# Optimization experiments

Hardware: AMD Instinct MI355X
Metric: run time of the kernel (lower is better)

## Reference

```python
import jax, jax.numpy as jnp
import numpy as np

N, E, G = 50000, 1600000, 512
H, NF_IN, NF_OUT, GF_OUT, EDIM, DEPTH = 128, 64, 64, 128, 16, 3
EPS = 1e-5


def seg_softmax(logits, seg, num):
    m = jax.ops.segment_max(logits, seg, num_segments=num)
    e = jnp.exp(logits - m[seg])
    s = jax.ops.segment_sum(e, seg, num_segments=num)
    return e / s[seg]


def batchnorm_train(x, gamma, beta):
    mu = jnp.mean(x, axis=0)
    var = jnp.mean((x - mu) ** 2, axis=0)  # biased, as torch BN training
    return (x - mu) * jax.lax.rsqrt(var + EPS) * gamma + beta


def setup_inputs() -> dict:
    key = jax.random.key(0)
    ks = jax.random.split(key, 20)
    inp = {}
    inp['x'] = jax.random.normal(ks[0], (N, NF_IN), jnp.float32)
    inp['edge_index'] = jax.random.randint(ks[1], (2, E), 0, N, jnp.int64)
    inp['edge_attr'] = jax.random.normal(ks[2], (E, EDIM), jnp.float32)
    inp['batch'] = jnp.sort(jax.random.randint(ks[3], (N,), 0, G, jnp.int64))
    inp['num_graphs'] = G
    s = 0.05
    inp['Wi'] = jax.random.normal(ks[4], (H, NF_IN), jnp.float32) * s
    inp['bi'] = jnp.zeros((H,), jnp.float32)
    inp['gat_W'] = jax.random.normal(ks[5], (DEPTH, H, 2 * H), jnp.float32) * s
    inp['gat_a'] = jax.random.normal(ks[6], (DEPTH, 2 * H), jnp.float32) * s
    inp['nfW1'] = jax.random.normal(ks[7], (H, H), jnp.float32) * s
    inp['nfb1'] = jnp.zeros((H,), jnp.float32)
    inp['nf_g'] = jnp.ones((H,), jnp.float32)
    inp['nf_b'] = jnp.zeros((H,), jnp.float32)
    inp['nfW2'] = jax.random.normal(ks[8], (NF_OUT, H), jnp.float32) * s
    inp['nfb2'] = jnp.zeros((NF_OUT,), jnp.float32)
    inp['gfW1'] = jax.random.normal(ks[9], (H, H), jnp.float32) * s
    inp['gfb1'] = jnp.zeros((H,), jnp.float32)
    inp['gf_g'] = jnp.ones((H,), jnp.float32)
    inp['gf_b'] = jnp.zeros((H,), jnp.float32)
    inp['gfW2'] = jax.random.normal(ks[10], (GF_OUT, H), jnp.float32) * s
    inp['gfb2'] = jnp.zeros((GF_OUT,), jnp.float32)
    return inp


def reference(x, edge_index, edge_attr, batch, num_graphs, Wi, bi, gat_W, gat_a,
              nfW1, nfb1, nf_g, nf_b, nfW2, nfb2,
              gfW1, gfb1, gf_g, gf_b, gfW2, gfb2):
    src, dst = edge_index[0], edge_index[1]
    nf = x @ Wi.T + bi  # [N,H]
    for i in range(DEPTH):
        src_nf = nf[src]            # [E,H]
        dst_nf = nf[dst]            # [E,H]
        ef = jnp.concatenate([src_nf, dst_nf], axis=-1) @ gat_a[i]  # [E]
        alpha = seg_softmax(ef, dst, N)
        agg = jax.ops.segment_sum(alpha[:, None] * src_nf, dst, num_segments=N)
        nf = jax.nn.relu(jnp.concatenate([nf, agg], axis=-1) @ gat_W[i].T)
    # 3-iteration attention pooling over graphs
    h = nf
    for _ in range(3):
        logits = jnp.sum(h * nf, axis=-1)  # [N]
        alpha = seg_softmax(logits, batch, num_graphs)
        h = alpha[:, None] * nf
    gf = jax.ops.segment_sum(h, batch, num_segments=num_graphs)  # [G,H]
    nf_out = jax.nn.relu(batchnorm_train(nf @ nfW1.T + nfb1, nf_g, nf_b)) @ nfW2.T + nfb2
    gf_out = jax.nn.relu(batchnorm_train(gf @ gfW1.T + gfb1, gf_g, gf_b)) @ gfW2.T + gfb2
    return nf_out, edge_attr, gf_out
```

## Files before the change

### kernel.cpp

```cpp
#include <hip/hip_runtime.h>

#define NN 50000
#define NE 1600000
#define NG 512
#define HD 128
#define NGRP 8
#define GRPSZ ((NN + NGRP - 1) / NGRP)
#define PCAP 28672

typedef __attribute__((ext_vector_type(8))) short bf16x8;
typedef __attribute__((ext_vector_type(4))) float f32x4;

static __device__ __forceinline__ unsigned bf16rn(float x) {
  unsigned b = __float_as_uint(x);
  return (b + 0x7FFFu + ((b >> 16) & 1u)) >> 16;
}
static __device__ __forceinline__ float bf16tof(unsigned short u) {
  return __uint_as_float(((unsigned)u) << 16);
}

__global__ void __launch_bounds__(256) k_part(const int* __restrict__ src,
                                              const int* __restrict__ dst,
                                              uint2* __restrict__ pairs,
                                              int* __restrict__ pcnt) {
  __shared__ uint2 buf[8][512];
  __shared__ int lcnt[8];
  __shared__ int gbase[8];
  __shared__ int nfl[8];
  const int tid = threadIdx.x;
  const int b = blockIdx.x & 7;
  if (tid < 8) lcnt[tid] = 0;
  __syncthreads();
  const int stride = gridDim.x * 256;
  for (int base_e = blockIdx.x * 256; base_e < NE; base_e += stride) {
    int e = base_e + tid;
    bool valid = e < NE;
    if (valid) {
      int d = dst[e];
      int s = src[e];
      int g = d / GRPSZ;
      int pos = atomicAdd(&lcnt[g], 1);
      buf[g][pos] = make_uint2((unsigned)d, (unsigned)s);
    }
    __syncthreads();
    if (tid < 8) {
      int c = lcnt[tid];
      int nf = (c >= 256) ? 256 : 0;
      nfl[tid] = nf;
      gbase[tid] = nf ? atomicAdd(&pcnt[tid * 8 + b], nf) : 0;
    }
    __syncthreads();
#pragma unroll
    for (int g0 = 0; g0 < 8; ++g0) {
      if (nfl[g0]) {
        int gb = gbase[g0] + tid;
        if (gb < PCAP)
          pairs[(size_t)(g0 * 8 + b) * PCAP + gb] = buf[g0][tid];
      }
    }
    __syncthreads();
#pragma unroll
    for (int g0 = 0; g0 < 8; ++g0) {
      if (nfl[g0]) {
        int rem = lcnt[g0] - 256;
        if (tid < rem) buf[g0][tid] = buf[g0][256 + tid];
      }
    }
    __syncthreads();
    if (tid < 8 && nfl[tid]) lcnt[tid] -= 256;
    __syncthreads();
  }
  if (tid < 8) {
    int c = lcnt[tid];
    gbase[tid] = c ? atomicAdd(&pcnt[tid * 8 + b], c) : 0;
  }
  __syncthreads();
#pragma unroll
  for (int g0 = 0; g0 < 8; ++g0) {
    int c = lcnt[g0];
    if (tid < c) {
      int gb = gbase[g0] + tid;
      if (gb < PCAP)
        pairs[(size_t)(g0 * 8 + b) * PCAP + gb] = buf[g0][tid];
    }
  }
}

__global__ void __launch_bounds__(256) k_hist(const uint2* __restrict__ pairs,
                                              const int* __restrict__ pcnt,
                                              int* __restrict__ hcnt) {
  __shared__ int hist[GRPSZ];
  const int b = blockIdx.x;
  const int g = b & 7, sub = b >> 3;
  const int li = g * 8 + sub;
  const int lo = g * GRPSZ;
  for (int i = threadIdx.x; i < GRPSZ; i += 256) hist[i] = 0;
  __syncthreads();
  int cnt = min(pcnt[li], PCAP);
  const uint2* lst = pairs + (size_t)li * PCAP;
  for (int i = threadIdx.x; i < cnt; i += 256)
    atomicAdd(&hist[(int)lst[i].x - lo], 1);
  __syncthreads();
  for (int i = threadIdx.x; i < GRPSZ; i += 256)
    hcnt[(size_t)li * GRPSZ + i] = hist[i];
}

__global__ void k_degsum(const int* __restrict__ hcnt, int* __restrict__ deg) {
  int d = blockIdx.x * 256 + threadIdx.x;
  if (d >= NN) return;
  int g = d / GRPSZ, i = d - g * GRPSZ;
  int s = 0;
#pragma unroll
  for (int sub = 0; sub < 8; ++sub) s += hcnt[(size_t)(g * 8 + sub) * GRPSZ + i];
  deg[d] = s;
}

__global__ void __launch_bounds__(256) k_scat3(const uint2* __restrict__ pairs,
                                               const int* __restrict__ pcnt,
                                               const int* __restrict__ hcnt,
                                               const int* __restrict__ row_ptr,
                                               int* __restrict__ csr_src) {
  __shared__ int cur[GRPSZ];
  const int b = blockIdx.x;
  const int g = b & 7, sub = b >> 3;
  const int li = g * 8 + sub;
  const int lo = g * GRPSZ;
  for (int i = threadIdx.x; i < GRPSZ; i += 256) {
    int base = row_ptr[lo + i];
    for (int s2 = 0; s2 < sub; ++s2)
      base += hcnt[(size_t)(g * 8 + s2) * GRPSZ + i];
    cur[i] = base;
  }
  __syncthreads();
  int cnt = min(pcnt[li], PCAP);
  const uint2* lst = pairs + (size_t)li * PCAP;
  for (int i = threadIdx.x; i < cnt; i += 256) {
    uint2 p = lst[i];
    int pos = atomicAdd(&cur[(int)p.x - lo], 1);
    csr_src[pos] = (int)p.y;
  }
}

__global__ void k_scan_block(const int* __restrict__ in, int* __restrict__ out,
                             int* __restrict__ bsum, int n) {
  __shared__ int tmp[1024];
  int i = blockIdx.x * 1024 + threadIdx.x;
  int v = (i < n) ? in[i] : 0;
  tmp[threadIdx.x] = v;
  __syncthreads();
  for (int off = 1; off < 1024; off <<= 1) {
    int t = (threadIdx.x >= (unsigned)off) ? tmp[threadIdx.x - off] : 0;
    __syncthreads();
    tmp[threadIdx.x] += t;
    __syncthreads();
  }
  if (i < n) out[i] = tmp[threadIdx.x] - v;
  if (threadIdx.x == 1023 && bsum) bsum[blockIdx.x] = tmp[1023];
}

__global__ void k_scan_small(int* __restrict__ a, int n) {
  __shared__ int tmp[1024];
  int v = ((int)threadIdx.x < n) ? a[threadIdx.x] : 0;
  tmp[threadIdx.x] = v;
  __syncthreads();
  for (int off = 1; off < 1024; off <<= 1) {
    int t = (threadIdx.x >= (unsigned)off) ? tmp[threadIdx.x - off] : 0;
    __syncthreads();
    tmp[threadIdx.x] += t;
    __syncthreads();
  }
  if ((int)threadIdx.x < n) a[threadIdx.x] = tmp[threadIdx.x] - v;
}

__global__ void k_scan_add(int* __restrict__ out, const int* __restrict__ bsum, int n) {
  int i = blockIdx.x * 1024 + threadIdx.x;
  if (i < n) out[i] += bsum[blockIdx.x];
  if (blockIdx.x == 0 && threadIdx.x == 0) out[n] = NE;
}

__global__ void k_init_bounds(int* __restrict__ gs, int* __restrict__ ge) {
  int g = blockIdx.x * 256 + threadIdx.x;
  if (g < NG) { gs[g] = NN; ge[g] = 0; }
}
__global__ void k_bounds(const int* __restrict__ batch, int* __restrict__ gs, int* __restrict__ ge) {
  int n = blockIdx.x * 256 + threadIdx.x;
  if (n < NN) {
    int b = batch[n];
    atomicMin(&gs[b], n);
    atomicMax(&ge[b], n + 1);
  }
}

__global__ void k_cvt(const float* __restrict__ a, unsigned short* __restrict__ b, int n) {
  int i = blockIdx.x * 256 + threadIdx.x;
  if (i < n) b[i] = (unsigned short)bf16rn(a[i]);
}

__global__ void k_gat_agg(const unsigned* __restrict__ nf16, const float* __restrict__ e1,
                          const int* __restrict__ row_ptr, const int* __restrict__ csr_src,
                          unsigned short* __restrict__ agg16) {
  int node = blockIdx.x * 4 + (threadIdx.x >> 6);
  int lane = threadIdx.x & 63;
  if (node >= NN) return;
  int s = row_ptr[node], e = row_ptr[node + 1];
  const int q = lane >> 4;
  const int c = lane & 15;

  float acc[8];
#pragma unroll
  for (int i = 0; i < 8; ++i) acc[i] = 0.f;
  float zloc = 0.f;

  int jj = s + q;
  bool v0 = jj < e;
  int sc = v0 ? csr_src[jj] : 0;
  float w = v0 ? e1[sc] : 0.f;
  uint4 u = *(const uint4*)(nf16 + (size_t)sc * 64 + c * 4);

  for (int j = s; j < e; j += 4) {
    int jn = j + 4 + q;
    bool vn = jn < e;
    int scn = vn ? csr_src[jn] : 0;
    float wn = vn ? e1[scn] : 0.f;
    uint4 un = *(const uint4*)(nf16 + (size_t)scn * 64 + c * 4);
    zloc += w;
    acc[0] = fmaf(w, __uint_as_float(u.x << 16), acc[0]);
    acc[1] = fmaf(w, __uint_as_float(u.x & 0xFFFF0000u), acc[1]);
    acc[2] = fmaf(w, __uint_as_float(u.y << 16), acc[2]);
    acc[3] = fmaf(w, __uint_as_float(u.y & 0xFFFF0000u), acc[3]);
    acc[4] = fmaf(w, __uint_as_float(u.z << 16), acc[4]);
    acc[5] = fmaf(w, __uint_as_float(u.z & 0xFFFF0000u), acc[5]);
    acc[6] = fmaf(w, __uint_as_float(u.w << 16), acc[6]);
    acc[7] = fmaf(w, __uint_as_float(u.w & 0xFFFF0000u), acc[7]);
    sc = scn; w = wn; u = un;
  }

  zloc += __shfl_xor(zloc, 16);
  zloc += __shfl_xor(zloc, 32);
  float inv = (zloc > 0.f) ? 1.f / zloc : 0.f;
#pragma unroll
  for (int i = 0; i < 8; ++i) {
    acc[i] += __shfl_xor(acc[i], 16);
    acc[i] += __shfl_xor(acc[i], 32);
    acc[i] *= inv;
  }
  if (q == 0) {
    uint4 pk;
    pk.x = bf16rn(acc[0]) | (bf16rn(acc[1]) << 16);
    pk.y = bf16rn(acc[2]) | (bf16rn(acc[3]) << 16);
    pk.z = bf16rn(acc[4]) | (bf16rn(acc[5]) << 16);
    pk.w = bf16rn(acc[6]) | (bf16rn(acc[7]) << 16);
    *(uint4*)(agg16 + (size_t)node * HD + c * 8) = pk;
  }
}

template <int K, int KA, int HO, bool RELUOUT, bool BIAS, bool OUTF32, bool OUT16, int DOTM>
__global__ void __launch_bounds__(256) k_mfma(
    const unsigned short* __restrict__ A1, const unsigned short* __restrict__ A2,
    const unsigned short* __restrict__ W16, const float* __restrict__ bias,
    float* __restrict__ outf, unsigned short* __restrict__ out16,
    const float* __restrict__ dvec, float* __restrict__ dout, int nrows) {
  constexpr int NT = HO / 16;
  const int l = threadIdx.x & 63;
  const int w = threadIdx.x >> 6;
  const int lr = l & 15;
  const int q = l >> 4;
  const int row0 = blockIdx.x * 64 + w * 16;
  const int arow = min(row0 + lr, nrows - 1);
  const unsigned short* pa1 = A1 + (size_t)arow * KA;
  const unsigned short* pa2 = (KA < K) ? (A2 + (size_t)arow * (K - KA)) : nullptr;

  f32x4 acc[NT];
#pragma unroll
  for (int t = 0; t < NT; ++t) acc[t] = (f32x4){0.f, 0.f, 0.f, 0.f};

#pragma unroll
  for (int s = 0; s < K / 32; ++s) {
    const int kg = s * 32 + q * 8;
    bf16x8 af;
    if constexpr (KA == K) {
      af = *(const bf16x8*)(pa1 + kg);
    } else {
      af = (s * 32 < KA) ? *(const bf16x8*)(pa1 + kg)
                         : *(const bf16x8*)(pa2 + (kg - KA));
    }
#pragma unroll
    for (int t = 0; t < NT; ++t) {
      bf16x8 bfr = *(const bf16x8*)(W16 + (size_t)(t * 16 + lr) * K + kg);
      acc[t] = __builtin_amdgcn_mfma_f32_16x16x32_bf16(af, bfr, acc[t], 0, 0, 0);
    }
  }

  float bv[BIAS ? NT : 1];
  if constexpr (BIAS) {
#pragma unroll
    for (int t = 0; t < NT; ++t) bv[t] = bias[t * 16 + lr];
  }
  float dv[DOTM == 1 ? NT : 1];
  if constexpr (DOTM == 1) {
#pragma unroll
    for (int t = 0; t < NT; ++t) dv[t] = dvec[t * 16 + lr];
  }
  float p[4] = {0.f, 0.f, 0.f, 0.f};
#pragma unroll
  for (int j = 0; j < 4; ++j) {
    int n = row0 + q * 4 + j;
    bool ok = n < nrows;
#pragma unroll
    for (int t = 0; t < NT; ++t) {
      float v = acc[t][j];
      if constexpr (BIAS) v += bv[t];
      if constexpr (RELUOUT) v = fmaxf(v, 0.f);
      if (ok) {
        if constexpr (OUTF32) outf[(size_t)n * HO + t * 16 + lr] = v;
        if constexpr (OUT16) out16[(size_t)n * HO + t * 16 + lr] = (unsigned short)bf16rn(v);
      }
      if constexpr (DOTM == 1) p[j] = fmaf(v, dv[t], p[j]);
      if constexpr (DOTM == 2) p[j] = fmaf(v, v, p[j]);
    }
  }
  if constexpr (DOTM != 0) {
#pragma unroll
    for (int j = 0; j < 4; ++j) {
      p[j] += __shfl_xor(p[j], 1);
      p[j] += __shfl_xor(p[j], 2);
      p[j] += __shfl_xor(p[j], 4);
      p[j] += __shfl_xor(p[j], 8);
    }
    if (lr == 0) {
#pragma unroll
      for (int j = 0; j < 4; ++j) {
        int n = row0 + q * 4 + j;
        if (n < nrows) dout[n] = (DOTM == 1) ? __expf(p[j]) : p[j];
      }
    }
  }
}

template <int K, int KA, int HO, bool PRE, bool RELUOUT, bool BIAS, bool OUT16, int DOTM>
__global__ void __launch_bounds__(256) k_gemm(
    const float* __restrict__ inA, const float* __restrict__ inB,
    const float* __restrict__ W, const float* __restrict__ bias,
    const float* __restrict__ preA, const float* __restrict__ preB,
    float* __restrict__ out, int nrows,
    unsigned* __restrict__ out16, const float* __restrict__ dvec,
    float* __restrict__ dout) {
  constexpr int KC = 64;
  constexpr int BM = 64;
  constexpr int MT = 4;
  constexpr int NT = HO / 16;
  constexpr int LDW = HO + 4;
  constexpr int LDA = KC + 4;

  __shared__ float Wl[KC * LDW];
  __shared__ float inl[BM * LDA];

  const int tid = threadIdx.x;
  const int tr = tid >> 4;
  const int tc = tid & 15;
  const int row0 = blockIdx.x * BM;
  const int r0 = tr * MT;
  const int c0 = tc * NT;

  float acc[MT][NT];
#pragma unroll
  for (int i = 0; i < MT; ++i)
#pragma unroll
    for (int j = 0; j < NT; ++j) acc[i][j] = BIAS ? bias[c0 + j] : 0.f;

  for (int cc = 0; cc < K / KC; ++cc) {
    const int k0 = cc * KC;
    if (cc) __syncthreads();
    for (int idx = tid; idx < HO * (KC / 4); idx += 256) {
      int h = idx >> 4;
      int qq = idx & 15;
      float4 w = *(const float4*)(W + (size_t)h * K + k0 + qq * 4);
      Wl[(qq * 4 + 0) * LDW + h] = w.x;
      Wl[(qq * 4 + 1) * LDW + h] = w.y;
      Wl[(qq * 4 + 2) * LDW + h] = w.z;
      Wl[(qq * 4 + 3) * LDW + h] = w.w;
    }
    for (int idx = tid; idx < BM * (KC / 4); idx += 256) {
      int r = idx >> 4;
      int qq = idx & 15;
      int n = row0 + r;
      int kg = k0 + qq * 4;
      float4 v = make_float4(0.f, 0.f, 0.f, 0.f);
      if (n < nrows) {
        if constexpr (KA == K) {
          v = *(const float4*)(inA + (size_t)n * K + kg);
        } else {
          if (k0 < KA) v = *(const float4*)(inA + (size_t)n * KA + kg);
          else         v = *(const float4*)(inB + (size_t)n * (K - KA) + kg - KA);
        }
      }
      if constexpr (PRE) {
        v.x = fmaxf(v.x * preA[kg + 0] + preB[kg + 0], 0.f);
        v.y = fmaxf(v.y * preA[kg + 1] + preB[kg + 1], 0.f);
        v.z = fmaxf(v.z * preA[kg + 2] + preB[kg + 2], 0.f);
        v.w = fmaxf(v.w * preA[kg + 3] + preB[kg + 3], 0.f);
      }
      *(float4*)(inl + r * LDA + qq * 4) = v;
    }
    __syncthreads();
#pragma unroll 8
    for (int k = 0; k < KC; ++k) {
      float a[MT];
#pragma unroll
      for (int i = 0; i < MT; ++i) a[i] = inl[(r0 + i) * LDA + k];
      float4 b0 = *(const float4*)(Wl + k * LDW + c0);
#pragma unroll
      for (int i = 0; i < MT; ++i) {
        acc[i][0] = fmaf(a[i], b0.x, acc[i][0]);
        acc[i][1] = fmaf(a[i], b0.y, acc[i][1]);
        acc[i][2] = fmaf(a[i], b0.z, acc[i][2]);
        acc[i][3] = fmaf(a[i], b0.w, acc[i][3]);
      }
      if constexpr (NT == 8) {
        float4 b1 = *(const float4*)(Wl + k * LDW + c0 + 4);
#pragma unroll
        for (int i = 0; i < MT; ++i) {
          acc[i][4] = fmaf(a[i], b1.x, acc[i][4]);
          acc[i][5] = fmaf(a[i], b1.y, acc[i][5]);
          acc[i][6] = fmaf(a[i], b1.z, acc[i][6]);
          acc[i][7] = fmaf(a[i], b1.w, acc[i][7]);
        }
      }
    }
  }
  float dv[DOTM == 1 ? NT : 1];
  if constexpr (DOTM == 1) {
#pragma unroll
    for (int j = 0; j < NT; ++j) dv[j] = dvec[c0 + j];
  }
#pragma unroll
  for (int i = 0; i < MT; ++i) {
    int n = row0 + r0 + i;
    if constexpr (RELUOUT) {
#pragma unroll
      for (int j = 0; j < NT; ++j) acc[i][j] = fmaxf(acc[i][j], 0.f);
    }
    if (n < nrows) {
      float4 o0 = make_float4(acc[i][0], acc[i][1], acc[i][2], acc[i][3]);
      *(float4*)(out + (size_t)n * HO + c0) = o0;
      if constexpr (NT == 8) {
        float4 o1 = make_float4(acc[i][4], acc[i][5], acc[i][6], acc[i][7]);
        *(float4*)(out + (size_t)n * HO + c0 + 4) = o1;
      }
      if constexpr (OUT16 && NT == 8) {
        uint4 pk;
        pk.x = bf16rn(acc[i][0]) | (bf16rn(acc[i][1]) << 16);
        pk.y = bf16rn(acc[i][2]) | (bf16rn(acc[i][3]) << 16);
        pk.z = bf16rn(acc[i][4]) | (bf16rn(acc[i][5]) << 16);
        pk.w = bf16rn(acc[i][6]) | (bf16rn(acc[i][7]) << 16);
        *(uint4*)(out16 + (size_t)n * 64 + tc * 4) = pk;
      }
    }
    if constexpr (DOTM != 0) {
      float p = 0.f;
#pragma unroll
      for (int j = 0; j < NT; ++j)
        p = fmaf(acc[i][j], (DOTM == 1) ? dv[j] : acc[i][j], p);
      p += __shfl_xor(p, 1);
      p += __shfl_xor(p, 2);
      p += __shfl_xor(p, 4);
      p += __shfl_xor(p, 8);
      if (tc == 0 && n < nrows) dout[n] = (DOTM == 1) ? __expf(p) : p;
    }
  }
}

__global__ void k_pool(const unsigned short* __restrict__ nf16, const float* __restrict__ r,
                       const int* __restrict__ gs, const int* __restrict__ ge,
                       float* __restrict__ alpha, float* __restrict__ gf) {
  int g = blockIdx.x;
  int s = gs[g], e = ge[g];
  __shared__ float red[256];
  for (int it = 0; it < 3; ++it) {
    float lm = -INFINITY;
    for (int n = s + threadIdx.x; n < e; n += 256) {
      float l = r[n];
      if (it) l *= alpha[n];
      lm = fmaxf(lm, l);
    }
    red[threadIdx.x] = lm;
    __syncthreads();
    for (int off = 128; off > 0; off >>= 1) {
      if ((int)threadIdx.x < off) red[threadIdx.x] = fmaxf(red[threadIdx.x], red[threadIdx.x + off]);
      __syncthreads();
    }
    float m = red[0];
    __syncthreads();
    float zz = 0.f;
    for (int n = s + threadIdx.x; n < e; n += 256) {
      float l = r[n];
      if (it) l *= alpha[n];
      zz += __expf(l - m);
    }
    red[threadIdx.x] = zz;
    __syncthreads();
    for (int off = 128; off > 0; off >>= 1) {
      if ((int)threadIdx.x < off) red[threadIdx.x] += red[threadIdx.x + off];
      __syncthreads();
    }
    float z = red[0];
    __syncthreads();
    float invz = 1.f / z;
    for (int n = s + threadIdx.x; n < e; n += 256) {
      float l = r[n];
      if (it) l *= alpha[n];
      alpha[n] = __expf(l - m) * invz;
    }
    __syncthreads();
  }
  int c = threadIdx.x & 127;
  int rr2 = threadIdx.x >> 7;
  float acc = 0.f;
  for (int n = s + rr2; n < e; n += 2)
    acc += alpha[n] * bf16tof(nf16[(size_t)n * HD + c]);
  red[threadIdx.x] = acc;
  __syncthreads();
  if (rr2 == 0) gf[(size_t)g * HD + c] = red[threadIdx.x] + red[threadIdx.x + 128];
}

__global__ void k_colstats(const float* __restrict__ y, float* __restrict__ sum,
                           float* __restrict__ sumsq, int R, int CH) {
  int c = threadIdx.x & 127;
  int rr = threadIdx.x >> 7;
  int r0 = blockIdx.x * CH;
  int r1 = min(R, r0 + CH);
  float s = 0.f, q = 0.f;
  for (int r = r0 + rr; r < r1; r += 2) {
    float v = y[(size_t)r * HD + c];
    s += v;
    q += v * v;
  }
  __shared__ float ls[256], lq[256];
  ls[threadIdx.x] = s;
  lq[threadIdx.x] = q;
  __syncthreads();
  if (rr == 0) {
    s += ls[threadIdx.x + 128];
    q += lq[threadIdx.x + 128];
    atomicAdd(&sum[c], s);
    atomicAdd(&sumsq[c], q);
  }
}

__global__ void k_bn_final(const float* __restrict__ sum, const float* __restrict__ sumsq,
                           const float* __restrict__ g, const float* __restrict__ b,
                           float* __restrict__ A, float* __restrict__ B, float R) {
  int c = threadIdx.x;
  float mu = sum[c] / R;
  float var = sumsq[c] / R - mu * mu;
  float a = g[c] * rsqrtf(var + 1e-5f);
  A[c] = a;
  B[c] = b[c] - mu * a;
}

__global__ void k_bnapply(const float* __restrict__ y, const float* __restrict__ Ac,
                          const float* __restrict__ Bc, unsigned short* __restrict__ z) {
  int i = blockIdx.x * 256 + threadIdx.x;
  if (i >= NN * 16) return;
  int c = (i & 15) * 8;
  const float4* yp = (const float4*)y + (size_t)i * 2;
  float4 v0 = yp[0], v1 = yp[1];
  float4 a0 = *(const float4*)(Ac + c), a1 = *(const float4*)(Ac + c + 4);
  float4 b0 = *(const float4*)(Bc + c), b1 = *(const float4*)(Bc + c + 4);
  float r0 = fmaxf(fmaf(v0.x, a0.x, b0.x), 0.f);
  float r1 = fmaxf(fmaf(v0.y, a0.y, b0.y), 0.f);
  float r2 = fmaxf(fmaf(v0.z, a0.z, b0.z), 0.f);
  float r3 = fmaxf(fmaf(v0.w, a0.w, b0.w), 0.f);
  float r4 = fmaxf(fmaf(v1.x, a1.x, b1.x), 0.f);
  float r5 = fmaxf(fmaf(v1.y, a1.y, b1.y), 0.f);
  float r6 = fmaxf(fmaf(v1.z, a1.z, b1.z), 0.f);
  float r7 = fmaxf(fmaf(v1.w, a1.w, b1.w), 0.f);
  uint4 pk;
  pk.x = bf16rn(r0) | (bf16rn(r1) << 16);
  pk.y = bf16rn(r2) | (bf16rn(r3) << 16);
  pk.z = bf16rn(r4) | (bf16rn(r5) << 16);
  pk.w = bf16rn(r6) | (bf16rn(r7) << 16);
  *(uint4*)(z + (size_t)i * 8) = pk;
}

__global__ void k_copy4(const float4* __restrict__ a, float4* __restrict__ b, int n) {
  int i = blockIdx.x * 256 + threadIdx.x;
  if (i < n) b[i] = a[i];
}

extern "C" void kernel_launch(void* const* d_in, const int* in_sizes, int n_in,
                              void* d_out, int out_size, void* d_ws, size_t ws_size,
                              hipStream_t stream) {
  const float* x        = (const float*)d_in[0];
  const int*   ei       = (const int*)d_in[1];
  const float* edge_attr= (const float*)d_in[2];
  const int*   batch    = (const int*)d_in[3];
  const float* Wi       = (const float*)d_in[5];
  const float* bi       = (const float*)d_in[6];
  const float* gat_W    = (const float*)d_in[7];
  const float* gat_a    = (const float*)d_in[8];
  const float* nfW1     = (const float*)d_in[9];
  const float* nfb1     = (const float*)d_in[10];
  const float* nf_g     = (const float*)d_in[11];
  const float* nf_b     = (const float*)d_in[12];
  const float* nfW2     = (const float*)d_in[13];
  const float* nfb2     = (const float*)d_in[14];
  const float* gfW1     = (const float*)d_in[15];
  const float* gfb1     = (const float*)d_in[16];
  const float* gf_g     = (const float*)d_in[17];
  const float* gf_b     = (const float*)d_in[18];
  const float* gfW2     = (const float*)d_in[19];
  const float* gfb2     = (const float*)d_in[20];

  float* out = (float*)d_out;

  unsigned short* nf16A = (unsigned short*)d_ws;
  unsigned short* nf16B = nf16A + (size_t)NN * HD;
  unsigned short* agg16 = nf16B + (size_t)NN * HD;
  unsigned short* z16   = agg16 + (size_t)NN * HD;
  unsigned short* wt_gat = z16 + (size_t)NN * HD;
  unsigned short* wt_nf1 = wt_gat + 3 * 128 * 256;
  unsigned short* wt_nf2 = wt_nf1 + 128 * 128;
  float* nfA   = (float*)(wt_nf2 + 64 * 128);
  float* e1v   = nfA + (size_t)NN * HD;
  float* rv    = e1v + NN;
  float* alpha = rv + NN;
  float* gf    = alpha + NN;
  float* gy    = gf + (size_t)NG * HD;
  float* sums  = gy + (size_t)NG * HD;
  int* deg     = (int*)(sums + 512);
  int* row_ptr = deg + NN;
  int* csr_src = row_ptr + NN + 1;
  int* bsum    = csr_src + NE;
  int* gs      = bsum + 64;
  int* ge      = gs + NG;
  int* pcnt    = ge + NG;
  int* hcnt    = pcnt + 64;
  uint2* pairs = (uint2*)nfA;

  const int* src  = ei;
  const int* dstp = ei + NE;

  hipMemsetAsync(pcnt, 0, 64 * sizeof(int), stream);
  k_part<<<512, 256, 0, stream>>>(src, dstp, pairs, pcnt);
  k_hist<<<64, 256, 0, stream>>>(pairs, pcnt, hcnt);
  k_degsum<<<(NN + 255) / 256, 256, 0, stream>>>(hcnt, deg);
  int nsb = (NN + 1023) / 1024;
  k_scan_block<<<nsb, 1024, 0, stream>>>(deg, row_ptr, bsum, NN);
  k_scan_small<<<1, 1024, 0, stream>>>(bsum, nsb);
  k_scan_add<<<nsb, 1024, 0, stream>>>(row_ptr, bsum, NN);
  k_scat3<<<64, 256, 0, stream>>>(pairs, pcnt, hcnt, row_ptr, csr_src);

  k_init_bounds<<<2, 256, 0, stream>>>(gs, ge);
  k_bounds<<<(NN + 255) / 256, 256, 0, stream>>>(batch, gs, ge);

  k_cvt<<<(3 * 128 * 256 + 255) / 256, 256, 0, stream>>>(gat_W, wt_gat, 3 * 128 * 256);
  k_cvt<<<(128 * 128 + 255) / 256, 256, 0, stream>>>(nfW1, wt_nf1, 128 * 128);
  k_cvt<<<(64 * 128 + 255) / 256, 256, 0, stream>>>(nfW2, wt_nf2, 64 * 128);

  k_gemm<64, 64, 128, false, false, true, true, 1><<<(NN + 63) / 64, 256, 0, stream>>>(
      x, nullptr, Wi, bi, nullptr, nullptr, nfA, NN, (unsigned*)nf16A, gat_a, e1v);

  unsigned short* cur = nf16A;
  unsigned short* nxt = nf16B;
  const int gemm_grid = (NN + 63) / 64;
  for (int l = 0; l < 3; ++l) {
    k_gat_agg<<<(NN + 3) / 4, 256, 0, stream>>>((const unsigned*)cur, e1v, row_ptr, csr_src, agg16);
    if (l < 2) {
      k_mfma<256, 128, 128, true, false, false, true, 1><<<gemm_grid, 256, 0, stream>>>(
          cur, agg16, wt_gat + (size_t)l * 128 * 256, nullptr,
          nullptr, nxt, gat_a + (size_t)(l + 1) * 256, e1v, NN);
    } else {
      k_mfma<256, 128, 128, true, false, false, true, 2><<<gemm_grid, 256, 0, stream>>>(
          cur, agg16, wt_gat + (size_t)l * 128 * 256, nullptr,
          nullptr, nxt, nullptr, rv, NN);
    }
    unsigned short* t = cur; cur = nxt; nxt = t;
  }

  k_pool<<<NG, 256, 0, stream>>>(cur, rv, gs, ge, alpha, gf);

  k_mfma<128, 128, 128, false, true, true, false, 0><<<gemm_grid, 256, 0, stream>>>(
      cur, nullptr, wt_nf1, nfb1, nfA, nullptr, nullptr, nullptr, NN);
  hipMemsetAsync(sums, 0, 256 * sizeof(float), stream);
  k_colstats<<<200, 256, 0, stream>>>(nfA, sums, sums + 128, NN, 250);
  k_bn_final<<<1, 128, 0, stream>>>(sums, sums + 128, nf_g, nf_b, sums + 256, sums + 384, (float)NN);
  k_bnapply<<<(NN * 16 + 255) / 256, 256, 0, stream>>>(nfA, sums + 256, sums + 384, z16);
  k_mfma<128, 128, 64, false, true, true, false, 0><<<gemm_grid, 256, 0, stream>>>(
      z16, nullptr, wt_nf2, nfb2, out, nullptr, nullptr, nullptr, NN);

  k_gemm<128, 128, 128, false, false, true, false, 0><<<(NG + 63) / 64, 256, 0, stream>>>(
      gf, nullptr, gfW1, gfb1, nullptr, nullptr, gy, NG, nullptr, nullptr, nullptr);
  hipMemsetAsync(sums, 0, 256 * sizeof(float), stream);
  k_colstats<<<4, 256, 0, stream>>>(gy, sums, sums + 128, NG, 128);
  k_bn_final<<<1, 128, 0, stream>>>(sums, sums + 128, gf_g, gf_b, sums + 256, sums + 384, (float)NG);
  k_gemm<128, 128, 128, true, false, true, false, 0><<<(NG + 63) / 64, 256, 0, stream>>>(
      gy, nullptr, gfW2, gfb2, sums + 256, sums + 384,
      out + (size_t)NN * 64 + (size_t)NE * 16, NG, nullptr, nullptr, nullptr);

  int n4 = NE * 16 / 4;
  k_copy4<<<(n4 + 255) / 256, 256, 0, stream>>>((const float4*)edge_attr,
                                                (float4*)(out + (size_t)NN * 64), n4);
}
```

Before: 674.0 us.

## Fuse CSR scan into scatter, merge weight conversions, widen GAT aggregation lanes

Replaces the degree-sum, three-stage scan and scatter kernels with one k_csr kernel. Each block computes its group's prefix offsets locally from pcnt and hcnt and writes row_ptr itself. The three weight conversion launches are merged into one kernel, and the separate BN sums memsets are folded into the single initial memset by giving the node and graph BN their own sum buffers. k_gat_agg now has each lane handle 16 features across 8 edges in parallel instead of 8 features across 4 edges, which raises memory-level parallelism per wave. The cost is more registers and some serial per-thread scanning work inside k_csr.

```diff
diff --git a/kernel.cpp b/kernel.cpp
--- a/kernel.cpp
+++ b/kernel.cpp
@@ -105,32 +105,55 @@
     hcnt[(size_t)li * GRPSZ + i] = hist[i];
 }
 
-__global__ void k_degsum(const int* __restrict__ hcnt, int* __restrict__ deg) {
-  int d = blockIdx.x * 256 + threadIdx.x;
-  if (d >= NN) return;
-  int g = d / GRPSZ, i = d - g * GRPSZ;
-  int s = 0;
-#pragma unroll
-  for (int sub = 0; sub < 8; ++sub) s += hcnt[(size_t)(g * 8 + sub) * GRPSZ + i];
-  deg[d] = s;
-}
-
-__global__ void __launch_bounds__(256) k_scat3(const uint2* __restrict__ pairs,
-                                               const int* __restrict__ pcnt,
-                                               const int* __restrict__ hcnt,
-                                               const int* __restrict__ row_ptr,
-                                               int* __restrict__ csr_src) {
+__global__ void __launch_bounds__(256) k_csr(const uint2* __restrict__ pairs,
+                                             const int* __restrict__ pcnt,
+                                             const int* __restrict__ hcnt,
+                                             int* __restrict__ row_ptr,
+                                             int* __restrict__ csr_src) {
+  __shared__ int rp[GRPSZ];
   __shared__ int cur[GRPSZ];
+  __shared__ int wsum[256];
   const int b = blockIdx.x;
   const int g = b & 7, sub = b >> 3;
   const int li = g * 8 + sub;
   const int lo = g * GRPSZ;
+  int gbase = 0;
+  for (int gg = 0; gg < g; ++gg)
+#pragma unroll
+    for (int ss = 0; ss < 8; ++ss) gbase += pcnt[gg * 8 + ss];
   for (int i = threadIdx.x; i < GRPSZ; i += 256) {
-    int base = row_ptr[lo + i];
-    for (int s2 = 0; s2 < sub; ++s2)
-      base += hcnt[(size_t)(g * 8 + s2) * GRPSZ + i];
-    cur[i] = base;
-  }
+    int dsum = 0, before = 0;
+#pragma unroll
+    for (int ss = 0; ss < 8; ++ss) {
+      int h = hcnt[(size_t)(g * 8 + ss) * GRPSZ + i];
+      dsum += h;
+      if (ss < sub) before += h;
+    }
+    rp[i] = dsum;
+    cur[i] = before;
+  }
+  __syncthreads();
+  const int CH = (GRPSZ + 255) / 256;
+  int t0 = threadIdx.x * CH;
+  int t1 = min(GRPSZ, t0 + CH);
+  int s = 0;
+  for (int i = t0; i < t1; ++i) { int v = rp[i]; rp[i] = s; s += v; }
+  wsum[threadIdx.x] = s;
+  __syncthreads();
+  for (int off = 1; off < 256; off <<= 1) {
+    int t = ((int)threadIdx.x >= off) ? wsum[threadIdx.x - off] : 0;
+    __syncthreads();
+    wsum[threadIdx.x] += t;
+    __syncthreads();
+  }
+  int add = gbase + ((threadIdx.x > 0) ? wsum[threadIdx.x - 1] : 0);
+  for (int i = t0; i < t1; ++i) rp[i] += add;
+  __syncthreads();
+  for (int i = threadIdx.x; i < GRPSZ; i += 256) {
+    cur[i] += rp[i];
+    if (sub == 0) row_ptr[lo + i] = rp[i];
+  }
+  if (sub == 0 && g == 7 && threadIdx.x == 0) row_ptr[NN] = NE;
   __syncthreads();
   int cnt = min(pcnt[li], PCAP);
   const uint2* lst = pairs + (size_t)li * PCAP;
@@ -141,43 +164,6 @@
   }
 }
 
-__global__ void k_scan_block(const int* __restrict__ in, int* __restrict__ out,
-                             int* __restrict__ bsum, int n) {
-  __shared__ int tmp[1024];
-  int i = blockIdx.x * 1024 + threadIdx.x;
-  int v = (i < n) ? in[i] : 0;
-  tmp[threadIdx.x] = v;
-  __syncthreads();
-  for (int off = 1; off < 1024; off <<= 1) {
-    int t = (threadIdx.x >= (unsigned)off) ? tmp[threadIdx.x - off] : 0;
-    __syncthreads();
-    tmp[threadIdx.x] += t;
-    __syncthreads();
-  }
-  if (i < n) out[i] = tmp[threadIdx.x] - v;
-  if (threadIdx.x == 1023 && bsum) bsum[blockIdx.x] = tmp[1023];
-}
-
-__global__ void k_scan_small(int* __restrict__ a, int n) {
-  __shared__ int tmp[1024];
-  int v = ((int)threadIdx.x < n) ? a[threadIdx.x] : 0;
-  tmp[threadIdx.x] = v;
-  __syncthreads();
-  for (int off = 1; off < 1024; off <<= 1) {
-    int t = (threadIdx.x >= (unsigned)off) ? tmp[threadIdx.x - off] : 0;
-    __syncthreads();
-    tmp[threadIdx.x] += t;
-    __syncthreads();
-  }
-  if ((int)threadIdx.x < n) a[threadIdx.x] = tmp[threadIdx.x] - v;
-}
-
-__global__ void k_scan_add(int* __restrict__ out, const int* __restrict__ bsum, int n) {
-  int i = blockIdx.x * 1024 + threadIdx.x;
-  if (i < n) out[i] += bsum[blockIdx.x];
-  if (blockIdx.x == 0 && threadIdx.x == 0) out[n] = NE;
-}
-
 __global__ void k_init_bounds(int* __restrict__ gs, int* __restrict__ ge) {
   int g = blockIdx.x * 256 + threadIdx.x;
   if (g < NG) { gs[g] = NN; ge[g] = 0; }
@@ -191,66 +177,89 @@
   }
 }
 
-__global__ void k_cvt(const float* __restrict__ a, unsigned short* __restrict__ b, int n) {
+__global__ void k_cvt3(const float* __restrict__ a0, int n0,
+                       const float* __restrict__ a1, int n1,
+                       const float* __restrict__ a2, int n2,
+                       unsigned short* __restrict__ b) {
   int i = blockIdx.x * 256 + threadIdx.x;
-  if (i < n) b[i] = (unsigned short)bf16rn(a[i]);
-}
-
-__global__ void k_gat_agg(const unsigned* __restrict__ nf16, const float* __restrict__ e1,
+  if (i >= n0 + n1 + n2) return;
+  float v = (i < n0) ? a0[i] : (i < n0 + n1) ? a1[i - n0] : a2[i - n0 - n1];
+  b[i] = (unsigned short)bf16rn(v);
+}
+
+__global__ void k_gat_agg(const uint4* __restrict__ nf16u4, const float* __restrict__ e1,
                           const int* __restrict__ row_ptr, const int* __restrict__ csr_src,
                           unsigned short* __restrict__ agg16) {
   int node = blockIdx.x * 4 + (threadIdx.x >> 6);
   int lane = threadIdx.x & 63;
   if (node >= NN) return;
   int s = row_ptr[node], e = row_ptr[node + 1];
-  const int q = lane >> 4;
-  const int c = lane & 15;
-
-  float acc[8];
-#pragma unroll
-  for (int i = 0; i < 8; ++i) acc[i] = 0.f;
+  const int q = lane >> 3;
+  const int c = lane & 7;
+
+  float acc[16];
+#pragma unroll
+  for (int i = 0; i < 16; ++i) acc[i] = 0.f;
   float zloc = 0.f;
 
   int jj = s + q;
   bool v0 = jj < e;
   int sc = v0 ? csr_src[jj] : 0;
   float w = v0 ? e1[sc] : 0.f;
-  uint4 u = *(const uint4*)(nf16 + (size_t)sc * 64 + c * 4);
-
-  for (int j = s; j < e; j += 4) {
-    int jn = j + 4 + q;
+  uint4 u0 = nf16u4[(size_t)sc * 16 + c * 2];
+  uint4 u1 = nf16u4[(size_t)sc * 16 + c * 2 + 1];
+
+  for (int j = s; j < e; j += 8) {
+    int jn = j + 8 + q;
     bool vn = jn < e;
     int scn = vn ? csr_src[jn] : 0;
     float wn = vn ? e1[scn] : 0.f;
-    uint4 un = *(const uint4*)(nf16 + (size_t)scn * 64 + c * 4);
+    uint4 un0 = nf16u4[(size_t)scn * 16 + c * 2];
+    uint4 un1 = nf16u4[(size_t)scn * 16 + c * 2 + 1];
     zloc += w;
-    acc[0] = fmaf(w, __uint_as_float(u.x << 16), acc[0]);
-    acc[1] = fmaf(w, __uint_as_float(u.x & 0xFFFF0000u), acc[1]);
-    acc[2] = fmaf(w, __uint_as_float(u.y << 16), acc[2]);
-    acc[3] = fmaf(w, __uint_as_float(u.y & 0xFFFF0000u), acc[3]);
-    acc[4] = fmaf(w, __uint_as_float(u.z << 16), acc[4]);
-    acc[5] = fmaf(w, __uint_as_float(u.z & 0xFFFF0000u), acc[5]);
-    acc[6] = fmaf(w, __uint_as_float(u.w << 16), acc[6]);
-    acc[7] = fmaf(w, __uint_as_float(u.w & 0xFFFF0000u), acc[7]);
-    sc = scn; w = wn; u = un;
-  }
-
+    acc[0]  = fmaf(w, __uint_as_float(u0.x << 16), acc[0]);
+    acc[1]  = fmaf(w, __uint_as_float(u0.x & 0xFFFF0000u), acc[1]);
+    acc[2]  = fmaf(w, __uint_as_float(u0.y << 16), acc[2]);
+    acc[3]  = fmaf(w, __uint_as_float(u0.y & 0xFFFF0000u), acc[3]);
+    acc[4]  = fmaf(w, __uint_as_float(u0.z << 16), acc[4]);
+    acc[5]  = fmaf(w, __uint_as_float(u0.z & 0xFFFF0000u), acc[5]);
+    acc[6]  = fmaf(w, __uint_as_float(u0.w << 16), acc[6]);
+    acc[7]  = fmaf(w, __uint_as_float(u0.w & 0xFFFF0000u), acc[7]);
+    acc[8]  = fmaf(w, __uint_as_float(u1.x << 16), acc[8]);
+    acc[9]  = fmaf(w, __uint_as_float(u1.x & 0xFFFF0000u), acc[9]);
+    acc[10] = fmaf(w, __uint_as_float(u1.y << 16), acc[10]);
+    acc[11] = fmaf(w, __uint_as_float(u1.y & 0xFFFF0000u), acc[11]);
+    acc[12] = fmaf(w, __uint_as_float(u1.z << 16), acc[12]);
+    acc[13] = fmaf(w, __uint_as_float(u1.z & 0xFFFF0000u), acc[13]);
+    acc[14] = fmaf(w, __uint_as_float(u1.w << 16), acc[14]);
+    acc[15] = fmaf(w, __uint_as_float(u1.w & 0xFFFF0000u), acc[15]);
+    sc = scn; w = wn; u0 = un0; u1 = un1;
+  }
+
+  zloc += __shfl_xor(zloc, 8);
   zloc += __shfl_xor(zloc, 16);
   zloc += __shfl_xor(zloc, 32);
   float inv = (zloc > 0.f) ? 1.f / zloc : 0.f;
 #pragma unroll
-  for (int i = 0; i < 8; ++i) {
+  for (int i = 0; i < 16; ++i) {
+    acc[i] += __shfl_xor(acc[i], 8);
     acc[i] += __shfl_xor(acc[i], 16);
     acc[i] += __shfl_xor(acc[i], 32);
     acc[i] *= inv;
   }
   if (q == 0) {
-    uint4 pk;
-    pk.x = bf16rn(acc[0]) | (bf16rn(acc[1]) << 16);
-    pk.y = bf16rn(acc[2]) | (bf16rn(acc[3]) << 16);
-    pk.z = bf16rn(acc[4]) | (bf16rn(acc[5]) << 16);
-    pk.w = bf16rn(acc[6]) | (bf16rn(acc[7]) << 16);
-    *(uint4*)(agg16 + (size_t)node * HD + c * 8) = pk;
+    uint4 p0, p1;
+    p0.x = bf16rn(acc[0])  | (bf16rn(acc[1])  << 16);
+    p0.y = bf16rn(acc[2])  | (bf16rn(acc[3])  << 16);
+    p0.z = bf16rn(acc[4])  | (bf16rn(acc[5])  << 16);
+    p0.w = bf16rn(acc[6])  | (bf16rn(acc[7])  << 16);
+    p1.x = bf16rn(acc[8])  | (bf16rn(acc[9])  << 16);
+    p1.y = bf16rn(acc[10]) | (bf16rn(acc[11]) << 16);
+    p1.z = bf16rn(acc[12]) | (bf16rn(acc[13]) << 16);
+    p1.w = bf16rn(acc[14]) | (bf16rn(acc[15]) << 16);
+    uint4* dst = (uint4*)(agg16 + (size_t)node * HD + c * 16);
+    dst[0] = p0;
+    dst[1] = p1;
   }
 }
 
@@ -627,36 +636,31 @@
   float* alpha = rv + NN;
   float* gf    = alpha + NN;
   float* gy    = gf + (size_t)NG * HD;
-  float* sums  = gy + (size_t)NG * HD;
-  int* deg     = (int*)(sums + 512);
-  int* row_ptr = deg + NN;
+  int*   pcnt  = (int*)(gy + (size_t)NG * HD);
+  float* sums  = (float*)(pcnt + 64);
+  float* sums2 = sums + 256;
+  float* bnAB  = sums2 + 256;
+  int* row_ptr = (int*)(bnAB + 256);
   int* csr_src = row_ptr + NN + 1;
-  int* bsum    = csr_src + NE;
-  int* gs      = bsum + 64;
+  int* gs      = csr_src + NE;
   int* ge      = gs + NG;
-  int* pcnt    = ge + NG;
-  int* hcnt    = pcnt + 64;
+  int* hcnt    = ge + NG;
   uint2* pairs = (uint2*)nfA;
 
   const int* src  = ei;
   const int* dstp = ei + NE;
 
-  hipMemsetAsync(pcnt, 0, 64 * sizeof(int), stream);
+  hipMemsetAsync(pcnt, 0, (64 + 512) * sizeof(int), stream);
+
   k_part<<<512, 256, 0, stream>>>(src, dstp, pairs, pcnt);
   k_hist<<<64, 256, 0, stream>>>(pairs, pcnt, hcnt);
-  k_degsum<<<(NN + 255) / 256, 256, 0, stream>>>(hcnt, deg);
-  int nsb = (NN + 1023) / 1024;
-  k_scan_block<<<nsb, 1024, 0, stream>>>(deg, row_ptr, bsum, NN);
-  k_scan_small<<<1, 1024, 0, stream>>>(bsum, nsb);
-  k_scan_add<<<nsb, 1024, 0, stream>>>(row_ptr, bsum, NN);
-  k_scat3<<<64, 256, 0, stream>>>(pairs, pcnt, hcnt, row_ptr, csr_src);
+  k_csr<<<64, 256, 0, stream>>>(pairs, pcnt, hcnt, row_ptr, csr_src);
 
   k_init_bounds<<<2, 256, 0, stream>>>(gs, ge);
   k_bounds<<<(NN + 255) / 256, 256, 0, stream>>>(batch, gs, ge);
 
-  k_cvt<<<(3 * 128 * 256 + 255) / 256, 256, 0, stream>>>(gat_W, wt_gat, 3 * 128 * 256);
-  k_cvt<<<(128 * 128 + 255) / 256, 256, 0, stream>>>(nfW1, wt_nf1, 128 * 128);
-  k_cvt<<<(64 * 128 + 255) / 256, 256, 0, stream>>>(nfW2, wt_nf2, 64 * 128);
+  k_cvt3<<<(3 * 128 * 256 + 128 * 128 + 64 * 128 + 255) / 256, 256, 0, stream>>>(
+      gat_W, 3 * 128 * 256, nfW1, 128 * 128, nfW2, 64 * 128, wt_gat);
 
   k_gemm<64, 64, 128, false, false, true, true, 1><<<(NN + 63) / 64, 256, 0, stream>>>(
       x, nullptr, Wi, bi, nullptr, nullptr, nfA, NN, (unsigned*)nf16A, gat_a, e1v);
@@ -665,7 +669,7 @@
   unsigned short* nxt = nf16B;
   const int gemm_grid = (NN + 63) / 64;
   for (int l = 0; l < 3; ++l) {
-    k_gat_agg<<<(NN + 3) / 4, 256, 0, stream>>>((const unsigned*)cur, e1v, row_ptr, csr_src, agg16);
+    k_gat_agg<<<(NN + 3) / 4, 256, 0, stream>>>((const uint4*)cur, e1v, row_ptr, csr_src, agg16);
     if (l < 2) {
       k_mfma<256, 128, 128, true, false, false, true, 1><<<gemm_grid, 256, 0, stream>>>(
           cur, agg16, wt_gat + (size_t)l * 128 * 256, nullptr,
@@ -682,20 +686,18 @@
 
   k_mfma<128, 128, 128, false, true, true, false, 0><<<gemm_grid, 256, 0, stream>>>(
       cur, nullptr, wt_nf1, nfb1, nfA, nullptr, nullptr, nullptr, NN);
-  hipMemsetAsync(sums, 0, 256 * sizeof(float), stream);
   k_colstats<<<200, 256, 0, stream>>>(nfA, sums, sums + 128, NN, 250);
-  k_bn_final<<<1, 128, 0, stream>>>(sums, sums + 128, nf_g, nf_b, sums + 256, sums + 384, (float)NN);
-  k_bnapply<<<(NN * 16 + 255) / 256, 256, 0, stream>>>(nfA, sums + 256, sums + 384, z16);
+  k_bn_final<<<1, 128, 0, stream>>>(sums, sums + 128, nf_g, nf_b, bnAB, bnAB + 128, (float)NN);
+  k_bnapply<<<(NN * 16 + 255) / 256, 256, 0, stream>>>(nfA, bnAB, bnAB + 128, z16);
   k_mfma<128, 128, 64, false, true, true, false, 0><<<gemm_grid, 256, 0, stream>>>(
       z16, nullptr, wt_nf2, nfb2, out, nullptr, nullptr, nullptr, NN);
 
   k_gemm<128, 128, 128, false, false, true, false, 0><<<(NG + 63) / 64, 256, 0, stream>>>(
       gf, nullptr, gfW1, gfb1, nullptr, nullptr, gy, NG, nullptr, nullptr, nullptr);
-  hipMemsetAsync(sums, 0, 256 * sizeof(float), stream);
-  k_colstats<<<4, 256, 0, stream>>>(gy, sums, sums + 128, NG, 128);
-  k_bn_final<<<1, 128, 0, stream>>>(sums, sums + 128, gf_g, gf_b, sums + 256, sums + 384, (float)NG);
+  k_colstats<<<4, 256, 0, stream>>>(gy, sums2, sums2 + 128, NG, 128);
+  k_bn_final<<<1, 128, 0, stream>>>(sums2, sums2 + 128, gf_g, gf_b, bnAB, bnAB + 128, (float)NG);
   k_gemm<128, 128, 128, true, false, true, false, 0><<<(NG + 63) / 64, 256, 0, stream>>>(
-      gy, nullptr, gfW2, gfb2, sums + 256, sums + 384,
+      gy, nullptr, gfW2, gfb2, bnAB, bnAB + 128,
       out + (size_t)NN * 64 + (size_t)NE * 16, NG, nullptr, nullptr, nullptr);
 
   int n4 = NE * 16 / 4;
```

Result: faster. 627.5 us (-6.9%).
